# Kernel optimization log

Hardware: AMD Instinct MI355X
Metric: run time of the kernel (lower is better)

The kernel has to match this reference:

```python
import jax, jax.numpy as jnp
import numpy as np

N_NODES = 2048


def setup_inputs() -> dict:
    key = jax.random.key(0)
    ks = jax.random.split(key, 10)
    s = 0.05
    return {
        "x": jax.random.normal(ks[0], (N_NODES, 32), dtype=jnp.float32),
        "centroids": jax.random.normal(ks[1], (N_NODES, 3), dtype=jnp.float32),
        "W_self1": jax.random.normal(ks[2], (35, 64), dtype=jnp.float32) * s,
        "W_neigh1": jax.random.normal(ks[3], (35, 64), dtype=jnp.float32) * s,
        "b1": jnp.zeros((64,), dtype=jnp.float32),
        "W_self2": jax.random.normal(ks[4], (64, 32), dtype=jnp.float32) * s,
        "W_neigh2": jax.random.normal(ks[5], (64, 32), dtype=jnp.float32) * s,
        "b2": jnp.zeros((32,), dtype=jnp.float32),
        "Wm1": jax.random.normal(ks[6], (64, 32), dtype=jnp.float32) * s,
        "bm1": jnp.zeros((32,), dtype=jnp.float32),
        "Wm2": jax.random.normal(ks[7], (32, 2), dtype=jnp.float32) * s,
        "bm2": jnp.zeros((2,), dtype=jnp.float32),
    }


def reference(x, centroids, W_self1, W_neigh1, b1, W_self2, W_neigh2, b2,
              Wm1, bm1, Wm2, bm2):
    n = x.shape[0]
    # Complete DAG edge list: edges i -> j for all i < j (static indices).
    src, dst = jnp.triu_indices(n, k=1)  # each [E], E = n(n-1)/2

    # --- edge features: per-feature cosine-sim vector + |centroid diff| ---
    norms = jnp.linalg.norm(x, axis=1)                       # [N]
    cos = (x[src] * x[dst]) / (norms[src] * norms[dst])[:, None]   # [E,32]
    cdiff = jnp.abs(centroids[src] - centroids[dst])               # [E,3]
    edge_weight = jnp.concatenate([cos, cdiff], axis=1)            # [E,35]

    h = jnp.concatenate([x, centroids], axis=1)                    # [N,35]

    # in-degree of each destination node (mean aggregator denominator)
    deg = jnp.zeros((n,), dtype=h.dtype).at[dst].add(1.0)
    inv_deg = jnp.where(deg > 0, 1.0 / jnp.maximum(deg, 1.0), 0.0)[:, None]

    # --- SAGEConv 1 (mean, with per-feature edge weights) ---
    msg1 = h[src] * edge_weight                                    # [E,35]
    neigh1 = jax.ops.segment_sum(msg1, dst, num_segments=n) * inv_deg
    h1 = h @ W_self1 + neigh1 @ W_neigh1 + b1                      # [N,64]

    # --- SAGEConv 2 (mean, no edge weight) ---
    neigh2 = jax.ops.segment_sum(h1[src], dst, num_segments=n) * inv_deg
    h2 = h1 @ W_self2 + neigh2 @ W_neigh2 + b2                     # [N,32]

    # --- pairwise edge gather + MLP head ---
    ef = jnp.concatenate([h2[src], h2[dst]], axis=1)               # [E,64]
    hid = jax.nn.relu(ef @ Wm1 + bm1)                              # [E,32]
    out = jax.nn.softmax(hid @ Wm2 + bm2, axis=-1)                 # [E,2]
    return out
```

## Files before the change

### kernel.cpp

```cpp
#include <hip/hip_runtime.h>
#include <math.h>

#define N_NODES 2048

__device__ __forceinline__ float invdeg(int j) { return j > 0 ? 1.0f / (float)j : 0.0f; }

__global__ __launch_bounds__(256) void k_edgefeat(const float* __restrict__ x,
                                                  const float* __restrict__ cent,
                                                  float* __restrict__ n1) {
  __shared__ float invn_s[N_NODES];
  __shared__ float sc[256];
  const int tid = threadIdx.x;
  const int bx = blockIdx.x;
  if (bx < 32) {
    const int f = bx;
    for (int r = 0; r < 8; ++r) {
      int n = tid + 256 * r;
      const float4* xp = (const float4*)(x + n * 32);
      float s = 0.f;
#pragma unroll
      for (int q = 0; q < 8; ++q) {
        float4 v = xp[q];
        s += v.x * v.x + v.y * v.y + v.z * v.z + v.w * v.w;
      }
      invn_s[n] = rsqrtf(s);
    }
    __syncthreads();
    float sv[8], xv[8];
    float ts = 0.f;
#pragma unroll
    for (int r = 0; r < 8; ++r) {
      int i = tid * 8 + r;
      float xf = x[i * 32 + f];
      xv[r] = xf;
      float s = xf * xf * invn_s[i];
      sv[r] = s;
      ts += s;
    }
    sc[tid] = ts;
    __syncthreads();
    for (int off = 1; off < 256; off <<= 1) {
      float v = (tid >= off) ? sc[tid - off] : 0.f;
      __syncthreads();
      sc[tid] += v;
      __syncthreads();
    }
    float P = sc[tid] - ts;
#pragma unroll
    for (int r = 0; r < 8; ++r) {
      int i = tid * 8 + r;
      n1[i * 35 + f] = P * xv[r] * invn_s[i] * invdeg(i);
      P += sv[r];
    }
  } else {
    const int j = (bx - 32) * 4 + (tid >> 6);
    const int lane = tid & 63;
    const float cj0 = cent[j * 3 + 0], cj1 = cent[j * 3 + 1], cj2 = cent[j * 3 + 2];
    float s0 = 0.f, s1 = 0.f, s2 = 0.f;
    for (int i = lane; i < j; i += 64) {
      float c0 = cent[i * 3 + 0], c1 = cent[i * 3 + 1], c2 = cent[i * 3 + 2];
      s0 += c0 * fabsf(c0 - cj0);
      s1 += c1 * fabsf(c1 - cj1);
      s2 += c2 * fabsf(c2 - cj2);
    }
#pragma unroll
    for (int d = 32; d > 0; d >>= 1) {
      s0 += __shfl_down(s0, d);
      s1 += __shfl_down(s1, d);
      s2 += __shfl_down(s2, d);
    }
    if (lane == 0) {
      float idg = invdeg(j);
      n1[j * 35 + 32] = s0 * idg;
      n1[j * 35 + 33] = s1 * idg;
      n1[j * 35 + 34] = s2 * idg;
    }
  }
}

__global__ __launch_bounds__(256) void k_h1(const float* __restrict__ x,
                                            const float* __restrict__ cent,
                                            const float* __restrict__ n1,
                                            const float* __restrict__ Ws1,
                                            const float* __restrict__ Wn1,
                                            const float* __restrict__ b1,
                                            float* __restrict__ h1) {
  const int tid = threadIdx.x;
  const int n = blockIdx.x * 4 + (tid >> 6);
  const int o = tid & 63;
  float acc = b1[o];
#pragma unroll
  for (int f = 0; f < 32; ++f)
    acc += x[n * 32 + f] * Ws1[f * 64 + o] + n1[n * 35 + f] * Wn1[f * 64 + o];
#pragma unroll
  for (int f = 32; f < 35; ++f)
    acc += cent[n * 3 + (f - 32)] * Ws1[f * 64 + o] + n1[n * 35 + f] * Wn1[f * 64 + o];
  h1[n * 64 + o] = acc;
}

__global__ __launch_bounds__(256) void k_scan_h1(const float* __restrict__ h1,
                                                 float* __restrict__ n2) {
  __shared__ float sc[256];
  const int tid = threadIdx.x;
  const int o = blockIdx.x;
  float sv[8];
  float ts = 0.f;
#pragma unroll
  for (int r = 0; r < 8; ++r) {
    int i = tid * 8 + r;
    float v = h1[i * 64 + o];
    sv[r] = v;
    ts += v;
  }
  sc[tid] = ts;
  __syncthreads();
  for (int off = 1; off < 256; off <<= 1) {
    float v = (tid >= off) ? sc[tid - off] : 0.f;
    __syncthreads();
    sc[tid] += v;
    __syncthreads();
  }
  float P = sc[tid] - ts;
#pragma unroll
  for (int r = 0; r < 8; ++r) {
    int i = tid * 8 + r;
    n2[i * 64 + o] = P * invdeg(i);
    P += sv[r];
  }
}

__global__ __launch_bounds__(256) void k_h2AB(const float* __restrict__ h1,
                                              const float* __restrict__ n2,
                                              const float* __restrict__ Ws2,
                                              const float* __restrict__ Wn2,
                                              const float* __restrict__ b2,
                                              const float* __restrict__ Wm1,
                                              const float* __restrict__ bm1,
                                              float* __restrict__ A,
                                              float* __restrict__ Bm) {
  __shared__ float h2s[8][32];
  const int tid = threadIdx.x;
  const int ln = tid >> 5;
  const int o = tid & 31;
  const int n = blockIdx.x * 8 + ln;
  float acc = b2[o];
#pragma unroll
  for (int f = 0; f < 64; ++f)
    acc += h1[n * 64 + f] * Ws2[f * 32 + o] + n2[n * 64 + f] * Wn2[f * 32 + o];
  h2s[ln][o] = acc;
  __syncthreads();
  float a = 0.f, b = bm1[o];
#pragma unroll
  for (int f = 0; f < 32; ++f) {
    float v = h2s[ln][f];
    a += v * Wm1[f * 32 + o];
    b += v * Wm1[(32 + f) * 32 + o];
  }
  A[n * 32 + o] = a;
  Bm[n * 32 + o] = b;
}

__global__ __launch_bounds__(256) void k_edges(const float* __restrict__ A,
                                               const float* __restrict__ Bm,
                                               const float* __restrict__ Wm2,
                                               const float* __restrict__ bm2,
                                               float2* __restrict__ out) {
  __shared__ float Bt[256 * 33];
  __shared__ float At[8 * 32];
  __shared__ float wm2s[64];
  __shared__ float bm2s[2];
  const int tid = threadIdx.x;
  const int j0 = blockIdx.x * 256;
  const int i0 = blockIdx.y * 8;
  if (i0 >= j0 + 255) return;
#pragma unroll
  for (int k = 0; k < 32; ++k) {
    int idx = tid + k * 256;
    int jj = idx >> 5, f = idx & 31;
    Bt[jj * 33 + f] = Bm[(j0 + jj) * 32 + f];
  }
  {
    int ii = tid >> 5, f = tid & 31;
    At[ii * 32 + f] = A[(i0 + ii) * 32 + f];
  }
  if (tid < 64) wm2s[tid] = Wm2[tid];
  if (tid < 2) bm2s[tid] = bm2[tid];
  __syncthreads();
  const int j = j0 + tid;
  float Br[32];
#pragma unroll
  for (int f = 0; f < 32; ++f) Br[f] = Bt[tid * 33 + f];
  const float bb0 = bm2s[0], bb1 = bm2s[1];
#pragma unroll
  for (int ii = 0; ii < 8; ++ii) {
    int i = i0 + ii;
    if (i >= j) continue;
    float l0 = bb0, l1 = bb1;
#pragma unroll
    for (int f = 0; f < 32; ++f) {
      float hv = At[ii * 32 + f] + Br[f];
      hv = fmaxf(hv, 0.f);
      l0 += hv * wm2s[f * 2];
      l1 += hv * wm2s[f * 2 + 1];
    }
    float t = __expf(l1 - l0);
    float p0 = 1.0f / (1.0f + t);
    float p1 = 1.0f - p0;
    int e = i * (2 * N_NODES - 1 - i) / 2 + (j - i - 1);
    out[e] = make_float2(p0, p1);
  }
}

extern "C" void kernel_launch(void* const* d_in, const int* in_sizes, int n_in,
                              void* d_out, int out_size, void* d_ws, size_t ws_size,
                              hipStream_t stream) {
  const float* x    = (const float*)d_in[0];
  const float* cent = (const float*)d_in[1];
  const float* Ws1  = (const float*)d_in[2];
  const float* Wn1  = (const float*)d_in[3];
  const float* b1   = (const float*)d_in[4];
  const float* Ws2  = (const float*)d_in[5];
  const float* Wn2  = (const float*)d_in[6];
  const float* b2   = (const float*)d_in[7];
  const float* Wm1  = (const float*)d_in[8];
  const float* bm1  = (const float*)d_in[9];
  const float* Wm2  = (const float*)d_in[10];
  const float* bm2  = (const float*)d_in[11];

  float* ws = (float*)d_ws;
  float* n1 = ws;
  float* h1 = n1 + 2048 * 35;
  float* n2 = h1 + 2048 * 64;
  float* A  = n2 + 2048 * 64;
  float* Bm = A + 2048 * 32;

  k_edgefeat<<<544, 256, 0, stream>>>(x, cent, n1);
  k_h1<<<512, 256, 0, stream>>>(x, cent, n1, Ws1, Wn1, b1, h1);
  k_scan_h1<<<64, 256, 0, stream>>>(h1, n2);
  k_h2AB<<<256, 256, 0, stream>>>(h1, n2, Ws2, Wn2, b2, Wm1, bm1, A, Bm);
  k_edges<<<dim3(8, 256), 256, 0, stream>>>(A, Bm, Wm2, bm2, (float2*)d_out);
}
```

Before: 138.4 us.

## Rework all kernels: LDS centroids, balanced pairing, padded n1, register-tiled edge MLP

The centroid edge-feature part now stages all centroids in LDS and has each wave handle two rows (j and 2047-j) to balance the triangular work. It launches 288 blocks instead of 544. The n1 row stride is padded to 36 so k_h1 can use float4 loads, and readfirstlane makes the node index uniform. k_h2AB splits the A and B projections across wave halves and launches 512 blocks. k_edges drops its LDS staging in favour of direct float4 loads of B and an f-outer loop with 8 accumulators, relying on scalar or cached loads of A and Wm2. The edge kernel, which writes the large output, is likely dominant.

Measured after the change: 128.0 us. -7.5%, faster.

```diff
diff --git a/kernel.cpp b/kernel.cpp
--- a/kernel.cpp
+++ b/kernel.cpp
@@ -2,17 +2,18 @@
 #include <math.h>
 
 #define N_NODES 2048
+#define N1S 36
 
 __device__ __forceinline__ float invdeg(int j) { return j > 0 ? 1.0f / (float)j : 0.0f; }
 
 __global__ __launch_bounds__(256) void k_edgefeat(const float* __restrict__ x,
                                                   const float* __restrict__ cent,
                                                   float* __restrict__ n1) {
-  __shared__ float invn_s[N_NODES];
-  __shared__ float sc[256];
   const int tid = threadIdx.x;
   const int bx = blockIdx.x;
   if (bx < 32) {
+    __shared__ float invn_s[N_NODES];
+    __shared__ float sc[256];
     const int f = bx;
     for (int r = 0; r < 8; ++r) {
       int n = tid + 256 * r;
@@ -49,31 +50,41 @@
 #pragma unroll
     for (int r = 0; r < 8; ++r) {
       int i = tid * 8 + r;
-      n1[i * 35 + f] = P * xv[r] * invn_s[i] * invdeg(i);
+      n1[i * N1S + f] = P * xv[r] * invn_s[i] * invdeg(i);
       P += sv[r];
     }
   } else {
-    const int j = (bx - 32) * 4 + (tid >> 6);
+    __shared__ float cs[N_NODES * 3];
+    const float4* cp = (const float4*)cent;
+    float4* csp = (float4*)cs;
+#pragma unroll
+    for (int q = 0; q < 6; ++q) csp[tid + 256 * q] = cp[tid + 256 * q];
+    __syncthreads();
+    const int w = (bx - 32) * 4 + (tid >> 6);
     const int lane = tid & 63;
-    const float cj0 = cent[j * 3 + 0], cj1 = cent[j * 3 + 1], cj2 = cent[j * 3 + 2];
-    float s0 = 0.f, s1 = 0.f, s2 = 0.f;
-    for (int i = lane; i < j; i += 64) {
-      float c0 = cent[i * 3 + 0], c1 = cent[i * 3 + 1], c2 = cent[i * 3 + 2];
-      s0 += c0 * fabsf(c0 - cj0);
-      s1 += c1 * fabsf(c1 - cj1);
-      s2 += c2 * fabsf(c2 - cj2);
-    }
-#pragma unroll
-    for (int d = 32; d > 0; d >>= 1) {
-      s0 += __shfl_down(s0, d);
-      s1 += __shfl_down(s1, d);
-      s2 += __shfl_down(s2, d);
-    }
-    if (lane == 0) {
-      float idg = invdeg(j);
-      n1[j * 35 + 32] = s0 * idg;
-      n1[j * 35 + 33] = s1 * idg;
-      n1[j * 35 + 34] = s2 * idg;
+#pragma unroll
+    for (int pick = 0; pick < 2; ++pick) {
+      const int j = pick ? (2047 - w) : w;
+      const float cj0 = cs[j * 3 + 0], cj1 = cs[j * 3 + 1], cj2 = cs[j * 3 + 2];
+      float s0 = 0.f, s1 = 0.f, s2 = 0.f;
+      for (int i = lane; i < j; i += 64) {
+        float c0 = cs[i * 3 + 0], c1 = cs[i * 3 + 1], c2 = cs[i * 3 + 2];
+        s0 += c0 * fabsf(c0 - cj0);
+        s1 += c1 * fabsf(c1 - cj1);
+        s2 += c2 * fabsf(c2 - cj2);
+      }
+#pragma unroll
+      for (int d = 32; d > 0; d >>= 1) {
+        s0 += __shfl_down(s0, d);
+        s1 += __shfl_down(s1, d);
+        s2 += __shfl_down(s2, d);
+      }
+      if (lane == 0) {
+        float idg = invdeg(j);
+        n1[j * N1S + 32] = s0 * idg;
+        n1[j * N1S + 33] = s1 * idg;
+        n1[j * N1S + 34] = s2 * idg;
+      }
     }
   }
 }
@@ -86,15 +97,27 @@
                                             const float* __restrict__ b1,
                                             float* __restrict__ h1) {
   const int tid = threadIdx.x;
-  const int n = blockIdx.x * 4 + (tid >> 6);
+  const int n = __builtin_amdgcn_readfirstlane(blockIdx.x * 4 + (tid >> 6));
   const int o = tid & 63;
   float acc = b1[o];
-#pragma unroll
-  for (int f = 0; f < 32; ++f)
-    acc += x[n * 32 + f] * Ws1[f * 64 + o] + n1[n * 35 + f] * Wn1[f * 64 + o];
-#pragma unroll
-  for (int f = 32; f < 35; ++f)
-    acc += cent[n * 3 + (f - 32)] * Ws1[f * 64 + o] + n1[n * 35 + f] * Wn1[f * 64 + o];
+  const float4* xr = (const float4*)(x + n * 32);
+  const float4* nr = (const float4*)(n1 + n * N1S);
+#pragma unroll
+  for (int q = 0; q < 8; ++q) {
+    float4 xv = xr[q];
+    float4 nv = nr[q];
+    acc += xv.x * Ws1[(4 * q + 0) * 64 + o] + nv.x * Wn1[(4 * q + 0) * 64 + o];
+    acc += xv.y * Ws1[(4 * q + 1) * 64 + o] + nv.y * Wn1[(4 * q + 1) * 64 + o];
+    acc += xv.z * Ws1[(4 * q + 2) * 64 + o] + nv.z * Wn1[(4 * q + 2) * 64 + o];
+    acc += xv.w * Ws1[(4 * q + 3) * 64 + o] + nv.w * Wn1[(4 * q + 3) * 64 + o];
+  }
+  {
+    float4 nv = nr[8];
+    float c0 = cent[n * 3 + 0], c1 = cent[n * 3 + 1], c2 = cent[n * 3 + 2];
+    acc += c0 * Ws1[32 * 64 + o] + nv.x * Wn1[32 * 64 + o];
+    acc += c1 * Ws1[33 * 64 + o] + nv.y * Wn1[33 * 64 + o];
+    acc += c2 * Ws1[34 * 64 + o] + nv.z * Wn1[34 * 64 + o];
+  }
   h1[n * 64 + o] = acc;
 }
 
@@ -138,26 +161,27 @@
                                               const float* __restrict__ bm1,
                                               float* __restrict__ A,
                                               float* __restrict__ Bm) {
-  __shared__ float h2s[8][32];
-  const int tid = threadIdx.x;
-  const int ln = tid >> 5;
-  const int o = tid & 31;
-  const int n = blockIdx.x * 8 + ln;
+  __shared__ float h2s[4][32];
+  const int tid = threadIdx.x;
+  const int wv = tid >> 6;
+  const int lane = tid & 63;
+  const int o = lane & 31;
+  const int half = lane >> 5;
+  const int n = __builtin_amdgcn_readfirstlane(blockIdx.x * 4 + wv);
   float acc = b2[o];
 #pragma unroll
   for (int f = 0; f < 64; ++f)
     acc += h1[n * 64 + f] * Ws2[f * 32 + o] + n2[n * 64 + f] * Wn2[f * 32 + o];
-  h2s[ln][o] = acc;
+  h2s[wv][o] = acc;
   __syncthreads();
-  float a = 0.f, b = bm1[o];
-#pragma unroll
-  for (int f = 0; f < 32; ++f) {
-    float v = h2s[ln][f];
-    a += v * Wm1[f * 32 + o];
-    b += v * Wm1[(32 + f) * 32 + o];
-  }
-  A[n * 32 + o] = a;
-  Bm[n * 32 + o] = b;
+  float r = half ? bm1[o] : 0.f;
+#pragma unroll
+  for (int f = 0; f < 32; ++f)
+    r += h2s[wv][f] * Wm1[(half * 32 + f) * 32 + o];
+  if (half)
+    Bm[n * 32 + o] = r;
+  else
+    A[n * 32 + o] = r;
 }
 
 __global__ __launch_bounds__(256) void k_edges(const float* __restrict__ A,
@@ -165,49 +189,47 @@
                                                const float* __restrict__ Wm2,
                                                const float* __restrict__ bm2,
                                                float2* __restrict__ out) {
-  __shared__ float Bt[256 * 33];
-  __shared__ float At[8 * 32];
-  __shared__ float wm2s[64];
-  __shared__ float bm2s[2];
   const int tid = threadIdx.x;
   const int j0 = blockIdx.x * 256;
   const int i0 = blockIdx.y * 8;
   if (i0 >= j0 + 255) return;
-#pragma unroll
-  for (int k = 0; k < 32; ++k) {
-    int idx = tid + k * 256;
-    int jj = idx >> 5, f = idx & 31;
-    Bt[jj * 33 + f] = Bm[(j0 + jj) * 32 + f];
-  }
-  {
-    int ii = tid >> 5, f = tid & 31;
-    At[ii * 32 + f] = A[(i0 + ii) * 32 + f];
-  }
-  if (tid < 64) wm2s[tid] = Wm2[tid];
-  if (tid < 2) bm2s[tid] = bm2[tid];
-  __syncthreads();
   const int j = j0 + tid;
   float Br[32];
-#pragma unroll
-  for (int f = 0; f < 32; ++f) Br[f] = Bt[tid * 33 + f];
-  const float bb0 = bm2s[0], bb1 = bm2s[1];
+  const float4* bp = (const float4*)(Bm + j * 32);
+#pragma unroll
+  for (int q = 0; q < 8; ++q) {
+    float4 v = bp[q];
+    Br[4 * q + 0] = v.x;
+    Br[4 * q + 1] = v.y;
+    Br[4 * q + 2] = v.z;
+    Br[4 * q + 3] = v.w;
+  }
+  const float bb0 = bm2[0], bb1 = bm2[1];
+  float l0[8], l1[8];
+#pragma unroll
+  for (int ii = 0; ii < 8; ++ii) {
+    l0[ii] = bb0;
+    l1[ii] = bb1;
+  }
+#pragma unroll
+  for (int f = 0; f < 32; ++f) {
+    const float w0 = Wm2[f * 2], w1 = Wm2[f * 2 + 1];
+    const float br = Br[f];
+#pragma unroll
+    for (int ii = 0; ii < 8; ++ii) {
+      float hv = fmaxf(A[(i0 + ii) * 32 + f] + br, 0.f);
+      l0[ii] += hv * w0;
+      l1[ii] += hv * w1;
+    }
+  }
 #pragma unroll
   for (int ii = 0; ii < 8; ++ii) {
     int i = i0 + ii;
     if (i >= j) continue;
-    float l0 = bb0, l1 = bb1;
-#pragma unroll
-    for (int f = 0; f < 32; ++f) {
-      float hv = At[ii * 32 + f] + Br[f];
-      hv = fmaxf(hv, 0.f);
-      l0 += hv * wm2s[f * 2];
-      l1 += hv * wm2s[f * 2 + 1];
-    }
-    float t = __expf(l1 - l0);
+    float t = __expf(l1[ii] - l0[ii]);
     float p0 = 1.0f / (1.0f + t);
-    float p1 = 1.0f - p0;
     int e = i * (2 * N_NODES - 1 - i) / 2 + (j - i - 1);
-    out[e] = make_float2(p0, p1);
+    out[e] = make_float2(p0, 1.0f - p0);
   }
 }
 
@@ -229,14 +251,14 @@
 
   float* ws = (float*)d_ws;
   float* n1 = ws;
-  float* h1 = n1 + 2048 * 35;
+  float* h1 = n1 + 2048 * N1S;
   float* n2 = h1 + 2048 * 64;
   float* A  = n2 + 2048 * 64;
   float* Bm = A + 2048 * 32;
 
-  k_edgefeat<<<544, 256, 0, stream>>>(x, cent, n1);
+  k_edgefeat<<<288, 256, 0, stream>>>(x, cent, n1);
   k_h1<<<512, 256, 0, stream>>>(x, cent, n1, Ws1, Wn1, b1, h1);
   k_scan_h1<<<64, 256, 0, stream>>>(h1, n2);
-  k_h2AB<<<256, 256, 0, stream>>>(h1, n2, Ws2, Wn2, b2, Wm1, bm1, A, Bm);
+  k_h2AB<<<512, 256, 0, stream>>>(h1, n2, Ws2, Wn2, b2, Wm1, bm1, A, Bm);
   k_edges<<<dim3(8, 256), 256, 0, stream>>>(A, Bm, Wm2, bm2, (float2*)d_out);
 }
```
